# Performance work log

Hardware: AMD Instinct MI355X
Metric: run time of the kernel (lower is better)

Reference implementation:

```python
import math
import jax, jax.numpy as jnp
import numpy as np

B, S, D, H = 4, 2048, 1024, 16
HD = D // H
SAMPLING_FACTOR = 5.0


def setup_inputs() -> dict:
    key = jax.random.key(0)
    ks = jax.random.split(key, 6)
    std = 1.0 / math.sqrt(D)
    inp = {
        "x": jax.random.normal(ks[0], (B, S, D), dtype=jnp.float32),
        "Wq": jax.random.normal(ks[1], (D, D), dtype=jnp.float32) * std,
        "bq": jnp.zeros((D,), dtype=jnp.float32),
        "Wk": jax.random.normal(ks[2], (D, D), dtype=jnp.float32) * std,
        "bk": jnp.zeros((D,), dtype=jnp.float32),
        "Wv": jax.random.normal(ks[3], (D, D), dtype=jnp.float32) * std,
        "bv": jnp.zeros((D,), dtype=jnp.float32),
        "Wo": jax.random.normal(ks[4], (D, D), dtype=jnp.float32) * std,
        "bo": jnp.zeros((D,), dtype=jnp.float32),
        "sample_idx": jax.random.randint(ks[5], (S,), 0, S, dtype=jnp.int32),
    }
    return inp


def reference(x, Wq, bq, Wk, bk, Wv, bv, Wo, bo, sample_idx):
    batch, seq_len, d_model = x.shape
    scale = math.sqrt(HD)
    # u = number of top (active) queries; U_part = seq_len here (sampling saturates)
    u = max(1, min(seq_len, int(SAMPLING_FACTOR * math.log(seq_len + 1))))

    def proj(W, b):
        # [B,S,D] -> [B,H,S,hd]
        return (x @ W + b).reshape(batch, seq_len, H, HD).transpose(0, 2, 1, 3)

    Q = proj(Wq, bq)
    K = proj(Wk, bk)
    V = proj(Wv, bv)

    # sparsity measure over sampled keys (with replacement)
    K_sample = K[:, :, sample_idx, :]                     # [B,H,U,hd]
    scores_sample = jnp.einsum("bhsd,bhud->bhsu", Q, K_sample) / scale
    M = scores_sample.max(axis=-1) - scores_sample.mean(axis=-1)  # [B,H,S]

    _, top_idx = jax.lax.top_k(M, u)                      # [B,H,u]

    Q_reduce = jnp.take_along_axis(Q, top_idx[..., None], axis=2)  # [B,H,u,hd]
    attn_scores = jnp.einsum("bhud,bhsd->bhus", Q_reduce, K) / scale
    attn_probs = jax.nn.softmax(attn_scores, axis=-1)
    context = jnp.einsum("bhus,bhsd->bhud", attn_probs, V)        # [B,H,u,hd]

    # fill lazy queries with mean of V, scatter active-query contexts
    V_mean = V.mean(axis=2, keepdims=True)                # [B,H,1,hd]
    out = jnp.broadcast_to(V_mean, (batch, H, seq_len, HD))
    b_idx = jnp.arange(batch)[:, None, None]
    h_idx = jnp.arange(H)[None, :, None]
    out = out.at[b_idx, h_idx, top_idx].set(context)      # [B,H,S,hd]

    out = out.transpose(0, 2, 1, 3).reshape(batch, seq_len, d_model)
    return out @ Wo + bo
```

## Files before the change

### kernel.cpp

```cpp
#include <hip/hip_runtime.h>
#include <math.h>
#include <stdint.h>
#include <stddef.h>

#define BB 4
#define SS 2048
#define DD 1024
#define HH 16
#define HD 64
#define UU 38
#define BH (BB*HH)
#define NROWS (BB*SS)
#define QSZ (BB*HH*SS*HD)
#define NSPLIT 4
#define SPLEN (SS/NSPLIT)
#define QPAD 40

typedef unsigned short ushortT;
typedef unsigned int u32;
typedef __attribute__((ext_vector_type(8))) short bf16x8;
typedef __attribute__((ext_vector_type(4))) float f32x4;

static __device__ __forceinline__ ushortT f2bf(float f) {
  union { float f; unsigned int u; } v; v.f = f;
  unsigned int r = v.u + 0x7fffu + ((v.u >> 16) & 1u);
  return (ushortT)(r >> 16);
}
static __device__ __forceinline__ float bf2f(ushortT h) {
  union { unsigned int u; float f; } v; v.u = ((unsigned int)h) << 16; return v.f;
}
static __device__ __forceinline__ void gld16(const void* g, void* l) {
  __builtin_amdgcn_global_load_lds((const __attribute__((address_space(1))) u32*)g,
                                   (__attribute__((address_space(3))) u32*)l, 16, 0, 0);
}

__global__ __launch_bounds__(256) void split_x(
    const float* __restrict__ x, ushortT* __restrict__ xh, ushortT* __restrict__ xl)
{
  size_t i = ((size_t)blockIdx.x * 256 + threadIdx.x) * 8;
  float4 v0 = *(const float4*)&x[i];
  float4 v1 = *(const float4*)&x[i + 4];
  float fv[8] = {v0.x, v0.y, v0.z, v0.w, v1.x, v1.y, v1.z, v1.w};
  bf16x8 hv, lv;
#pragma unroll
  for (int j = 0; j < 8; ++j) {
    ushortT h = f2bf(fv[j]);
    hv[j] = (short)h;
    lv[j] = (short)f2bf(fv[j] - bf2f(h));
  }
  *(bf16x8*)&xh[i] = hv;
  *(bf16x8*)&xl[i] = lv;
}

__global__ __launch_bounds__(256) void splitT_kernel(
    const float* __restrict__ W, ushortT* __restrict__ WhT, ushortT* __restrict__ WlT)
{
  __shared__ float tile[64][65];
  const int t = threadIdx.x;
  const int bk = blockIdx.y * 64, bn = blockIdx.x * 64;
  const int rr = t >> 4, c4 = (t & 15) * 4;
#pragma unroll
  for (int p = 0; p < 4; ++p) {
    int row = rr + p * 16;
    float4 v = *(const float4*)&W[(size_t)(bk + row) * DD + bn + c4];
    tile[row][c4] = v.x; tile[row][c4+1] = v.y; tile[row][c4+2] = v.z; tile[row][c4+3] = v.w;
  }
  __syncthreads();
  const int n = t & 63, ks = (t >> 6) * 16;
  union { ushortT us[16]; uint4 q[2]; } hb, lb;
#pragma unroll
  for (int j = 0; j < 16; ++j) {
    float f = tile[ks + j][n];
    ushortT h = f2bf(f);
    hb.us[j] = h;
    lb.us[j] = f2bf(f - bf2f(h));
  }
  size_t o = ((size_t)(bn + n) * DD + (size_t)(bk + ks)) >> 3;
  ((uint4*)WhT)[o] = hb.q[0]; ((uint4*)WhT)[o + 1] = hb.q[1];
  ((uint4*)WlT)[o] = lb.q[0]; ((uint4*)WlT)[o + 1] = lb.q[1];
}

__global__ __launch_bounds__(256) void dedupe_kernel(
    const int* __restrict__ sidx, int* __restrict__ uidx, int* __restrict__ ucount)
{
  __shared__ unsigned bm[64];
  __shared__ int base[64];
  const int t = threadIdx.x;
  if (t < 64) bm[t] = 0;
  __syncthreads();
  for (int s = t; s < SS; s += 256) {
    int v = sidx[s];
    atomicOr(&bm[v >> 5], 1u << (v & 31));
  }
  __syncthreads();
  if (t < 64) {
    int c = __popc(bm[t]);
    int pre = c;
#pragma unroll
    for (int off = 1; off < 64; off <<= 1) {
      int o = __shfl_up(pre, off, 64);
      if (t >= off) pre += o;
    }
    base[t] = pre - c;
    if (t == 63) ucount[0] = pre;
  }
  __syncthreads();
  if (t < 64) {
    unsigned m = bm[t];
    int o = base[t];
    while (m) {
      int b = __ffs(m) - 1;
      uidx[o++] = t * 32 + b;
      m &= m - 1;
    }
  }
  __syncthreads();
  int total = ucount[0];
  int padded = (total + 127) & ~127;
  int first = uidx[0];
  for (int i = total + t; i < padded; i += 256) uidx[i] = first;
}

template<bool EMIT_B16, bool EMIT_F32>
__global__ __launch_bounds__(256, 3) void gemm_mfma(
    const ushortT* __restrict__ Axh, const ushortT* __restrict__ Axl,
    const ushortT* __restrict__ BhT, const ushortT* __restrict__ BlT,
    const float* __restrict__ bias,
    float* __restrict__ outF, ushortT* __restrict__ outH, ushortT* __restrict__ outL)
{
  __shared__ ushortT As[128 * 64];
  __shared__ ushortT Bs[128 * 64];
  const int t = threadIdx.x;
  const int lin = blockIdx.x;
  const int swz = (lin & 7) * 64 + (lin >> 3);
  const int m0 = (swz >> 3) * 128;
  const int n0 = (swz & 7) * 128;
  const int lane = t & 63, w = t >> 6;
  const int wr = w >> 1, wc = w & 1;
  const int fr = lane & 15, fs = lane >> 4;
  const int srow = t >> 3, sslot = t & 7;
  f32x4 acc[4][4];
#pragma unroll
  for (int i = 0; i < 4; ++i)
#pragma unroll
    for (int j = 0; j < 4; ++j) acc[i][j] = (f32x4){0.f, 0.f, 0.f, 0.f};

  for (int kt = 0; kt < 48; ++kt) {
    const int seg = kt >> 4;
    const int rk0 = (kt & 15) * 64;
    const ushortT* a_src = (seg == 1) ? Axl : Axh;
    const ushortT* b_src = (seg == 2) ? BlT : BhT;
    __syncthreads();
#pragma unroll
    for (int is = 0; is < 4; ++is) {
      int row = is * 32 + srow;
      int soff = ((sslot ^ (row & 7)) * 8);
      int cb = (is * 256 + (t & 192)) * 8;
      gld16(&a_src[(size_t)(m0 + row) * DD + rk0 + soff], &As[cb]);
      gld16(&b_src[(size_t)(n0 + row) * DD + rk0 + soff], &Bs[cb]);
    }
    __syncthreads();
#pragma unroll
    for (int kk = 0; kk < 2; ++kk) {
      bf16x8 af[4], bf[4];
#pragma unroll
      for (int i = 0; i < 4; ++i) {
        int row = wr * 64 + i * 16 + fr;
        af[i] = *(const bf16x8*)&As[row * 64 + (((kk * 4 + fs) ^ (row & 7)) * 8)];
      }
#pragma unroll
      for (int j = 0; j < 4; ++j) {
        int row = wc * 64 + j * 16 + fr;
        bf[j] = *(const bf16x8*)&Bs[row * 64 + (((kk * 4 + fs) ^ (row & 7)) * 8)];
      }
#pragma unroll
      for (int i = 0; i < 4; ++i)
#pragma unroll
        for (int j = 0; j < 4; ++j)
          acc[i][j] = __builtin_amdgcn_mfma_f32_16x16x32_bf16(af[i], bf[j], acc[i][j], 0, 0, 0);
    }
  }
#pragma unroll
  for (int i = 0; i < 4; ++i) {
#pragma unroll
    for (int j = 0; j < 4; ++j) {
      int c = n0 + wc * 64 + j * 16 + fr;
      float bs = bias[c];
      int h = c >> 6, hd = c & 63;
#pragma unroll
      for (int r = 0; r < 4; ++r) {
        int m = m0 + wr * 64 + i * 16 + fs * 4 + r;
        int b = m >> 11, s = m & (SS - 1);
        size_t oidx = (((size_t)(b * HH + h)) * SS + s) * HD + hd;
        float val = acc[i][j][r] + bs;
        if (EMIT_F32) outF[oidx] = val;
        if (EMIT_B16) {
          ushortT hv = f2bf(val);
          outH[oidx] = hv;
          outL[oidx] = f2bf(val - bf2f(hv));
        }
      }
    }
  }
}

__global__ __launch_bounds__(256) void means_kernel(
    const float* __restrict__ K, const float* __restrict__ V,
    const int* __restrict__ sidx,
    float* __restrict__ Kmean, float* __restrict__ Vmean)
{
  __shared__ float rk[4][64], rv[4][64];
  const int bh = blockIdx.x;
  const int t = threadIdx.x;
  const int d = t & 63, p = t >> 6;
  const float* Kb = K + (size_t)bh * SS * HD;
  const float* Vb = V + (size_t)bh * SS * HD;
  float ka = 0.f, va = 0.f;
  for (int r = p * 512; r < (p + 1) * 512; ++r) {
    ka += Kb[(size_t)sidx[r] * HD + d];
    va += Vb[(size_t)r * HD + d];
  }
  rk[p][d] = ka; rv[p][d] = va;
  __syncthreads();
  if (t < 64) {
    Kmean[bh * HD + t] = (rk[0][t] + rk[1][t] + rk[2][t] + rk[3][t]) * (1.0f / SS);
    Vmean[bh * HD + t] = (rv[0][t] + rv[1][t] + rv[2][t] + rv[3][t]) * (1.0f / SS);
  }
}

__global__ __launch_bounds__(256, 2) void m_mfma(
    const ushortT* __restrict__ Qhg, const ushortT* __restrict__ Qlg,
    const ushortT* __restrict__ Khg, const ushortT* __restrict__ Klg,
    const int* __restrict__ uidx, const int* __restrict__ ucount,
    const float* __restrict__ Kmean, float* __restrict__ M)
{
  __shared__ ushortT QhL[128 * 64], QlL[128 * 64], KhL[128 * 64], KlL[128 * 64];
  __shared__ float Mred[2][128];
  __shared__ float km[64];
  const int t = threadIdx.x;
  const int lin = blockIdx.x;
  const int swz = (lin & 7) * 128 + (lin >> 3);
  const int bh = swz >> 4;
  const int s0 = (swz & 15) * 128;
  const int lane = t & 63, w = t >> 6;
  const int wr = w >> 1, wc = w & 1;
  const int fr = lane & 15, fs = lane >> 4;
  if (t < 64) km[t] = Kmean[bh * HD + t];
  const int srow = t >> 3, sslot = t & 7;
  const int ntiles = (ucount[0] + 127) >> 7;
#pragma unroll
  for (int is = 0; is < 4; ++is) {
    int row = is * 32 + srow;
    int soff = ((sslot ^ (row & 7)) * 8);
    int cb = (is * 256 + (t & 192)) * 8;
    size_t ga = ((size_t)bh * SS + s0 + row) * HD + soff;
    gld16(&Qhg[ga], &QhL[cb]);
    gld16(&Qlg[ga], &QlL[cb]);
  }
  float runmax[4][4];
#pragma unroll
  for (int i = 0; i < 4; ++i)
#pragma unroll
    for (int r = 0; r < 4; ++r) runmax[i][r] = -INFINITY;

  for (int ui = 0; ui < ntiles; ++ui) {
    __syncthreads();
#pragma unroll
    for (int is = 0; is < 4; ++is) {
      int row = is * 32 + srow;
      int gr = uidx[ui * 128 + row];
      int soff = ((sslot ^ (row & 7)) * 8);
      int cb = (is * 256 + (t & 192)) * 8;
      size_t ga = ((size_t)bh * SS + gr) * HD + soff;
      gld16(&Khg[ga], &KhL[cb]);
      gld16(&Klg[ga], &KlL[cb]);
    }
    __syncthreads();
    f32x4 acc[4][4];
#pragma unroll
    for (int i = 0; i < 4; ++i)
#pragma unroll
      for (int j = 0; j < 4; ++j) acc[i][j] = (f32x4){0.f, 0.f, 0.f, 0.f};
#pragma unroll
    for (int kk = 0; kk < 2; ++kk) {
      bf16x8 ah[4], al[4], bh[4], bl[4];
#pragma unroll
      for (int i = 0; i < 4; ++i) {
        int row = wr * 64 + i * 16 + fr;
        int off = row * 64 + (((kk * 4 + fs) ^ (row & 7)) * 8);
        ah[i] = *(const bf16x8*)&QhL[off];
        al[i] = *(const bf16x8*)&QlL[off];
      }
#pragma unroll
      for (int j = 0; j < 4; ++j) {
        int row = wc * 64 + j * 16 + fr;
        int off = row * 64 + (((kk * 4 + fs) ^ (row & 7)) * 8);
        bh[j] = *(const bf16x8*)&KhL[off];
        bl[j] = *(const bf16x8*)&KlL[off];
      }
#pragma unroll
      for (int i = 0; i < 4; ++i)
#pragma unroll
        for (int j = 0; j < 4; ++j) {
          acc[i][j] = __builtin_amdgcn_mfma_f32_16x16x32_bf16(ah[i], bh[j], acc[i][j], 0, 0, 0);
          acc[i][j] = __builtin_amdgcn_mfma_f32_16x16x32_bf16(ah[i], bl[j], acc[i][j], 0, 0, 0);
          acc[i][j] = __builtin_amdgcn_mfma_f32_16x16x32_bf16(al[i], bh[j], acc[i][j], 0, 0, 0);
        }
    }
#pragma unroll
    for (int i = 0; i < 4; ++i)
#pragma unroll
      for (int j = 0; j < 4; ++j)
#pragma unroll
        for (int r = 0; r < 4; ++r) runmax[i][r] = fmaxf(runmax[i][r], acc[i][j][r]);
  }
#pragma unroll
  for (int i = 0; i < 4; ++i)
#pragma unroll
    for (int r = 0; r < 4; ++r) {
      float v = runmax[i][r];
      v = fmaxf(v, __shfl_xor(v, 1, 64));
      v = fmaxf(v, __shfl_xor(v, 2, 64));
      v = fmaxf(v, __shfl_xor(v, 4, 64));
      v = fmaxf(v, __shfl_xor(v, 8, 64));
      runmax[i][r] = v;
    }
  if (fr == 0) {
#pragma unroll
    for (int i = 0; i < 4; ++i)
#pragma unroll
      for (int r = 0; r < 4; ++r)
        Mred[wc][wr * 64 + i * 16 + fs * 4 + r] = runmax[i][r];
  }
  __syncthreads();
  if (t < 128) {
    float mx = fmaxf(Mred[0][t], Mred[1][t]);
    float md = 0.f;
    const ushortT* qh = &Qhg[((size_t)bh * SS + s0 + t) * HD];
    const ushortT* ql = &Qlg[((size_t)bh * SS + s0 + t) * HD];
#pragma unroll
    for (int k8 = 0; k8 < 8; ++k8) {
      bf16x8 hv = *(const bf16x8*)&qh[k8 * 8];
      bf16x8 lv = *(const bf16x8*)&ql[k8 * 8];
#pragma unroll
      for (int j = 0; j < 8; ++j)
        md += (bf2f((ushortT)hv[j]) + bf2f((ushortT)lv[j])) * km[k8 * 8 + j];
    }
    M[(size_t)bh * SS + s0 + t] = (mx - md) * 0.125f;
  }
}

__global__ __launch_bounds__(256) void topk_kernel(const float* __restrict__ M,
                                                   int* __restrict__ topi)
{
  __shared__ float rw[4];
  __shared__ int   ri4[4];
  __shared__ int   winner;
  const int t = threadIdx.x, bh = blockIdx.x;
  const int lane = t & 63, w = t >> 6;
  float v[8];
#pragma unroll
  for (int j = 0; j < 8; ++j) v[j] = M[(size_t)bh * SS + t + j * 256];
  for (int it = 0; it < UU; ++it) {
    float bv = v[0]; int bj = 0;
#pragma unroll
    for (int j = 1; j < 8; ++j) if (v[j] > bv) { bv = v[j]; bj = j; }
    int bs = t + bj * 256;
#pragma unroll
    for (int off = 32; off > 0; off >>= 1) {
      float ov = __shfl_xor(bv, off, 64);
      int os = __shfl_xor(bs, off, 64);
      if (ov > bv || (ov == bv && os < bs)) { bv = ov; bs = os; }
    }
    if (lane == 0) { rw[w] = bv; ri4[w] = bs; }
    __syncthreads();
    if (t == 0) {
      float fv = rw[0]; int fsx = ri4[0];
#pragma unroll
      for (int g = 1; g < 4; ++g)
        if (rw[g] > fv || (rw[g] == fv && ri4[g] < fsx)) { fv = rw[g]; fsx = ri4[g]; }
      topi[bh * UU + it] = fsx;
      winner = fsx;
    }
    __syncthreads();
    int wi = winner;
    if ((wi & 255) == t) {
      int jj = wi >> 8;
#pragma unroll
      for (int j = 0; j < 8; ++j) if (j == jj) v[j] = -INFINITY;
    }
  }
}

__global__ __launch_bounds__(256) void attn_flash(
    const ushortT* __restrict__ Qhg, const ushortT* __restrict__ Qlg,
    const float* __restrict__ K, const float* __restrict__ V,
    const int* __restrict__ topi,
    float* __restrict__ pacc, float* __restrict__ pm, float* __restrict__ pl)
{
  __shared__ float Qt[64][68];
  __shared__ float KV[64][68];
  __shared__ float Ps[64][68];
  __shared__ float redA[16][64];
  __shared__ float redB[16][64];
  __shared__ float mrow[64], lrow[64], scl[64];
  const int t  = threadIdx.x;
  const int bh = blockIdx.x;
  const int sp = blockIdx.y;
  const float* Kb = K + (size_t)bh * SS * HD;
  const float* Vb = V + (size_t)bh * SS * HD;
  if (t < 64) { mrow[t] = -INFINITY; lrow[t] = 0.f; }
  {
    int q = t >> 2, k4 = (t & 3) * 16;
    float fv[16];
#pragma unroll
    for (int e = 0; e < 16; ++e) fv[e] = 0.f;
    if (q < UU) {
      int qidx = topi[bh * UU + q];
      size_t ga = ((size_t)bh * SS + qidx) * HD + k4;
      bf16x8 h0 = *(const bf16x8*)&Qhg[ga];
      bf16x8 h1 = *(const bf16x8*)&Qhg[ga + 8];
      bf16x8 l0 = *(const bf16x8*)&Qlg[ga];
      bf16x8 l1 = *(const bf16x8*)&Qlg[ga + 8];
#pragma unroll
      for (int j = 0; j < 8; ++j) {
        fv[j]     = bf2f((ushortT)h0[j]) + bf2f((ushortT)l0[j]);
        fv[8 + j] = bf2f((ushortT)h1[j]) + bf2f((ushortT)l1[j]);
      }
    }
#pragma unroll
    for (int e = 0; e < 16; ++e) Qt[k4 + e][q] = fv[e];
  }
  const int q4 = (t & 15) * 4, j4g = (t >> 4) * 4, d4 = (t >> 4) * 4;
  const int lj = t >> 2, lk4 = (t & 3) * 16;
  float acc[4][4] = {};
  for (int s0 = sp * SPLEN; s0 < (sp + 1) * SPLEN; s0 += 64) {
    __syncthreads();
#pragma unroll
    for (int i = 0; i < 4; ++i) {
      float4 v = *(const float4*)&Kb[(size_t)(s0 + lj) * HD + lk4 + 4 * i];
      KV[lk4 + 4*i + 0][lj] = v.x; KV[lk4 + 4*i + 1][lj] = v.y;
      KV[lk4 + 4*i + 2][lj] = v.z; KV[lk4 + 4*i + 3][lj] = v.w;
    }
    __syncthreads();
    float sacc[4][4] = {};
#pragma unroll 16
    for (int k = 0; k < 64; ++k) {
      float4 a = *(const float4*)&Qt[k][q4];
      float4 b = *(const float4*)&KV[k][j4g];
      sacc[0][0] += a.x*b.x; sacc[0][1] += a.x*b.y; sacc[0][2] += a.x*b.z; sacc[0][3] += a.x*b.w;
      sacc[1][0] += a.y*b.x; sacc[1][1] += a.y*b.y; sacc[1][2] += a.y*b.z; sacc[1][3] += a.y*b.w;
      sacc[2][0] += a.z*b.x; sacc[2][1] += a.z*b.y; sacc[2][2] += a.z*b.z; sacc[2][3] += a.z*b.w;
      sacc[3][0] += a.w*b.x; sacc[3][1] += a.w*b.y; sacc[3][2] += a.w*b.z; sacc[3][3] += a.w*b.w;
    }
#pragma unroll
    for (int i = 0; i < 4; ++i) {
      float mx = fmaxf(fmaxf(sacc[i][0], sacc[i][1]), fmaxf(sacc[i][2], sacc[i][3]));
      redA[t >> 4][q4 + i] = mx;
    }
    __syncthreads();
    if (t < 64) {
      float mx = redA[0][t];
#pragma unroll
      for (int g = 1; g < 16; ++g) mx = fmaxf(mx, redA[g][t]);
      float mn = fmaxf(mrow[t], mx * 0.125f);
      scl[t] = __expf(mrow[t] - mn);
      mrow[t] = mn;
    }
    __syncthreads();
    float4 vld[4];
#pragma unroll
    for (int i = 0; i < 4; ++i)
      vld[i] = *(const float4*)&Vb[(size_t)(s0 + lj) * HD + lk4 + 4 * i];
    float psum[4] = {};
#pragma unroll
    for (int i = 0; i < 4; ++i) {
#pragma unroll
      for (int j = 0; j < 4; ++j) {
        float e = __expf(sacc[i][j] * 0.125f - mrow[q4 + i]);
        Ps[j4g + j][q4 + i] = e;
        psum[i] += e;
      }
      redB[t >> 4][q4 + i] = psum[i];
    }
#pragma unroll
    for (int i = 0; i < 4; ++i)
      *(float4*)&KV[lj][lk4 + 4 * i] = vld[i];
    __syncthreads();
    if (t < 64) {
      float ts = redB[0][t];
#pragma unroll
      for (int g = 1; g < 16; ++g) ts += redB[g][t];
      lrow[t] = lrow[t] * scl[t] + ts;
    }
#pragma unroll
    for (int i = 0; i < 4; ++i) {
      float fsc = scl[q4 + i];
      acc[i][0] *= fsc; acc[i][1] *= fsc; acc[i][2] *= fsc; acc[i][3] *= fsc;
    }
#pragma unroll 16
    for (int j = 0; j < 64; ++j) {
      float4 a = *(const float4*)&Ps[j][q4];
      float4 b = *(const float4*)&KV[j][d4];
      acc[0][0] += a.x*b.x; acc[0][1] += a.x*b.y; acc[0][2] += a.x*b.z; acc[0][3] += a.x*b.w;
      acc[1][0] += a.y*b.x; acc[1][1] += a.y*b.y; acc[1][2] += a.y*b.z; acc[1][3] += a.y*b.w;
      acc[2][0] += a.z*b.x; acc[2][1] += a.z*b.y; acc[2][2] += a.z*b.z; acc[2][3] += a.z*b.w;
      acc[3][0] += a.w*b.x; acc[3][1] += a.w*b.y; acc[3][2] += a.w*b.z; acc[3][3] += a.w*b.w;
    }
  }
  const size_t pb = ((size_t)bh * NSPLIT + sp) * QPAD;
#pragma unroll
  for (int i = 0; i < 4; ++i) {
    int q = q4 + i;
    if (q < UU) {
#pragma unroll
      for (int j = 0; j < 4; ++j)
        pacc[(pb + q) * HD + d4 + j] = acc[i][j];
    }
  }
  if (t < UU) { pm[pb + t] = mrow[t]; pl[pb + t] = lrow[t]; }
}

__global__ __launch_bounds__(256) void attn_combine(
    const float* __restrict__ pacc, const float* __restrict__ pm,
    const float* __restrict__ pl, float* __restrict__ ctx)
{
  const int t  = threadIdx.x;
  const int bh = blockIdx.x;
  const int d = t & 63, qg = t >> 6;
  for (int q = qg; q < UU; q += 4) {
    float m0 = pm[((size_t)bh * NSPLIT + 0) * QPAD + q];
    float m1 = pm[((size_t)bh * NSPLIT + 1) * QPAD + q];
    float m2 = pm[((size_t)bh * NSPLIT + 2) * QPAD + q];
    float m3 = pm[((size_t)bh * NSPLIT + 3) * QPAD + q];
    float ms = fmaxf(fmaxf(m0, m1), fmaxf(m2, m3));
    float w0 = __expf(m0 - ms), w1 = __expf(m1 - ms), w2 = __expf(m2 - ms), w3 = __expf(m3 - ms);
    float l = w0 * pl[((size_t)bh * NSPLIT + 0) * QPAD + q]
            + w1 * pl[((size_t)bh * NSPLIT + 1) * QPAD + q]
            + w2 * pl[((size_t)bh * NSPLIT + 2) * QPAD + q]
            + w3 * pl[((size_t)bh * NSPLIT + 3) * QPAD + q];
    float c = w0 * pacc[(((size_t)bh * NSPLIT + 0) * QPAD + q) * HD + d]
            + w1 * pacc[(((size_t)bh * NSPLIT + 1) * QPAD + q) * HD + d]
            + w2 * pacc[(((size_t)bh * NSPLIT + 2) * QPAD + q) * HD + d]
            + w3 * pacc[(((size_t)bh * NSPLIT + 3) * QPAD + q) * HD + d];
    ctx[((size_t)bh * UU + q) * HD + d] = c / l;
  }
}

__global__ void base_kernel(const float* __restrict__ Vmean, const float* __restrict__ Wo,
                            const float* __restrict__ bo, float* __restrict__ base)
{
  const int c = blockIdx.x * 256 + threadIdx.x;
  float acc[BB] = {};
  for (int k = 0; k < DD; ++k) {
    float w = Wo[(size_t)k * DD + c];
#pragma unroll
    for (int b = 0; b < BB; ++b) acc[b] += Vmean[b * DD + k] * w;
  }
#pragma unroll
  for (int b = 0; b < BB; ++b) base[b * DD + c] = acc[b] + bo[c];
}

__global__ void fill_kernel(const float* __restrict__ base, float* __restrict__ out)
{
  size_t i = (size_t)blockIdx.x * 256 + threadIdx.x;
  float4 bv = ((const float4*)base)[(i >> 19) * 256 + (i & 255)];
  ((float4*)out)[i] = bv;
}

__global__ __launch_bounds__(256) void scatter_kernel(
    const float* __restrict__ ctx, const float* __restrict__ Vmean,
    const int* __restrict__ topi, const float* __restrict__ Wo,
    float* __restrict__ out)
{
  __shared__ float delta[64];
  const int t  = threadIdx.x;
  const int bh = blockIdx.x;
  const int u  = blockIdx.y;
  const int b = bh >> 4, h = bh & 15;
  const int s = topi[bh * UU + u];
  if (t < 64) delta[t] = ctx[((size_t)bh * UU + u) * HD + t] - Vmean[bh * HD + t];
  __syncthreads();
  float* orow = out + ((size_t)b * SS + s) * DD;
#pragma unroll
  for (int j = 0; j < 4; ++j) {
    int c = t + j * 256;
    float acc = 0.f;
#pragma unroll 8
    for (int d = 0; d < 64; ++d) acc += delta[d] * Wo[(size_t)(h * HD + d) * DD + c];
    atomicAdd(&orow[c], acc);
  }
}

extern "C" void kernel_launch(void* const* d_in, const int* in_sizes, int n_in,
                              void* d_out, int out_size, void* d_ws, size_t ws_size,
                              hipStream_t stream) {
  const float* x  = (const float*)d_in[0];
  const float* Wq = (const float*)d_in[1];
  const float* bq = (const float*)d_in[2];
  const float* Wk = (const float*)d_in[3];
  const float* bk = (const float*)d_in[4];
  const float* Wv = (const float*)d_in[5];
  const float* bv = (const float*)d_in[6];
  const float* Wo = (const float*)d_in[7];
  const float* bo = (const float*)d_in[8];
  const int* sidx = (const int*)d_in[9];
  float* out = (float*)d_out;

  float* f     = (float*)d_ws;
  float* K     = f;
  float* V     = f + (size_t)QSZ;
  float* Kmean = f + (size_t)2 * QSZ;
  float* Vmean = Kmean + BH * HD;
  float* Mbuf  = Vmean + BH * HD;
  float* base  = Mbuf + (size_t)BH * SS;
  float* ctx   = base + BB * DD;
  float* pacc  = ctx + (size_t)BH * UU * HD;
  float* pm    = pacc + (size_t)BH * NSPLIT * QPAD * HD;
  float* pl    = pm + (size_t)BH * NSPLIT * QPAD;
  int*   topi  = (int*)(pl + (size_t)BH * NSPLIT * QPAD);
  int*   uidx  = topi + 4096;
  int*   ucount= uidx + 4096;
  ushortT* usp = (ushortT*)(ucount + 64);
  ushortT* WqhT = usp;
  ushortT* WqlT = WqhT + (size_t)DD * DD;
  ushortT* WkhT = WqlT + (size_t)DD * DD;
  ushortT* WklT = WkhT + (size_t)DD * DD;
  ushortT* WvhT = WklT + (size_t)DD * DD;
  ushortT* WvlT = WvhT + (size_t)DD * DD;
  ushortT* xh   = WvlT + (size_t)DD * DD;
  ushortT* xl   = xh + (size_t)NROWS * DD;
  ushortT* Qhg  = xl + (size_t)NROWS * DD;
  ushortT* Qlg  = Qhg + (size_t)QSZ;
  ushortT* Khg  = Qlg + (size_t)QSZ;
  ushortT* Klg  = Khg + (size_t)QSZ;

  split_x<<<NROWS * DD / (256 * 8), 256, 0, stream>>>(x, xh, xl);
  dim3 gs(16, 16);
  splitT_kernel<<<gs, 256, 0, stream>>>(Wq, WqhT, WqlT);
  splitT_kernel<<<gs, 256, 0, stream>>>(Wk, WkhT, WklT);
  splitT_kernel<<<gs, 256, 0, stream>>>(Wv, WvhT, WvlT);
  dedupe_kernel<<<1, 256, 0, stream>>>(sidx, uidx, ucount);
  gemm_mfma<true, false><<<512, 256, 0, stream>>>(xh, xl, WqhT, WqlT, bq, nullptr, Qhg, Qlg);
  gemm_mfma<true, true ><<<512, 256, 0, stream>>>(xh, xl, WkhT, WklT, bk, K, Khg, Klg);
  gemm_mfma<false, true><<<512, 256, 0, stream>>>(xh, xl, WvhT, WvlT, bv, V, nullptr, nullptr);
  means_kernel<<<BH, 256, 0, stream>>>(K, V, sidx, Kmean, Vmean);
  m_mfma<<<1024, 256, 0, stream>>>(Qhg, Qlg, Khg, Klg, uidx, ucount, Kmean, Mbuf);
  topk_kernel<<<BH, 256, 0, stream>>>(Mbuf, topi);
  attn_flash<<<dim3(BH, NSPLIT), 256, 0, stream>>>(Qhg, Qlg, K, V, topi, pacc, pm, pl);
  attn_combine<<<BH, 256, 0, stream>>>(pacc, pm, pl, ctx);
  base_kernel<<<DD / 256, 256, 0, stream>>>(Vmean, Wo, bo, base);
  fill_kernel<<<(NROWS * DD / 4) / 256, 256, 0, stream>>>(base, out);
  scatter_kernel<<<dim3(BH, UU), 256, 0, stream>>>(ctx, Vmean, topi, Wo, out);
}
```

Before: 473.3 us.

## Fuse QKV GEMMs, drop fp32 K, split attention finer, parallelize base GEMV

The three projection GEMM launches become a single 1536-block kernel that selects weights, bias and output by tile index. K is no longer written in fp32; the means and attention kernels rebuild it from the bf16 hi/lo pair, which saves one large fp32 write. The attention split count goes from 4 to 8 for more blocks, with a generic combine loop. The base GEMV now splits the k-loop across threads and reduces through shared memory, giving 64 blocks instead of 4.

New measurement: 474.8 us. No clear change (+0.3%).

```diff
diff --git a/kernel.cpp b/kernel.cpp
--- a/kernel.cpp
+++ b/kernel.cpp
@@ -12,7 +12,7 @@
 #define BH (BB*HH)
 #define NROWS (BB*SS)
 #define QSZ (BB*HH*SS*HD)
-#define NSPLIT 4
+#define NSPLIT 8
 #define SPLEN (SS/NSPLIT)
 #define QPAD 40
 
@@ -121,20 +121,28 @@
   for (int i = total + t; i < padded; i += 256) uidx[i] = first;
 }
 
-template<bool EMIT_B16, bool EMIT_F32>
-__global__ __launch_bounds__(256, 3) void gemm_mfma(
+__global__ __launch_bounds__(256, 3) void gemm_qkv(
     const ushortT* __restrict__ Axh, const ushortT* __restrict__ Axl,
-    const ushortT* __restrict__ BhT, const ushortT* __restrict__ BlT,
-    const float* __restrict__ bias,
-    float* __restrict__ outF, ushortT* __restrict__ outH, ushortT* __restrict__ outL)
+    const ushortT* __restrict__ WqhT, const ushortT* __restrict__ WqlT,
+    const ushortT* __restrict__ WkhT, const ushortT* __restrict__ WklT,
+    const ushortT* __restrict__ WvhT, const ushortT* __restrict__ WvlT,
+    const float* __restrict__ bq, const float* __restrict__ bk, const float* __restrict__ bv,
+    ushortT* __restrict__ Qhg, ushortT* __restrict__ Qlg,
+    ushortT* __restrict__ Khg, ushortT* __restrict__ Klg,
+    float* __restrict__ V)
 {
   __shared__ ushortT As[128 * 64];
   __shared__ ushortT Bs[128 * 64];
   const int t = threadIdx.x;
   const int lin = blockIdx.x;
-  const int swz = (lin & 7) * 64 + (lin >> 3);
-  const int m0 = (swz >> 3) * 128;
-  const int n0 = (swz & 7) * 128;
+  const int swz = (lin & 7) * 192 + (lin >> 3);
+  const int n_idx = swz >> 6;
+  const int m0 = (swz & 63) * 128;
+  const int p = n_idx >> 3;
+  const int n0 = (n_idx & 7) * 128;
+  const ushortT* Bh = (p == 0) ? WqhT : (p == 1) ? WkhT : WvhT;
+  const ushortT* Bl = (p == 0) ? WqlT : (p == 1) ? WklT : WvlT;
+  const float* bias = (p == 0) ? bq : (p == 1) ? bk : bv;
   const int lane = t & 63, w = t >> 6;
   const int wr = w >> 1, wc = w & 1;
   const int fr = lane & 15, fs = lane >> 4;
@@ -149,7 +157,7 @@
     const int seg = kt >> 4;
     const int rk0 = (kt & 15) * 64;
     const ushortT* a_src = (seg == 1) ? Axl : Axh;
-    const ushortT* b_src = (seg == 2) ? BlT : BhT;
+    const ushortT* b_src = (seg == 2) ? Bl : Bh;
     __syncthreads();
 #pragma unroll
     for (int is = 0; is < 4; ++is) {
@@ -193,11 +201,13 @@
         int b = m >> 11, s = m & (SS - 1);
         size_t oidx = (((size_t)(b * HH + h)) * SS + s) * HD + hd;
         float val = acc[i][j][r] + bs;
-        if (EMIT_F32) outF[oidx] = val;
-        if (EMIT_B16) {
+        if (p == 2) {
+          V[oidx] = val;
+        } else {
           ushortT hv = f2bf(val);
-          outH[oidx] = hv;
-          outL[oidx] = f2bf(val - bf2f(hv));
+          ushortT lv = f2bf(val - bf2f(hv));
+          if (p == 0) { Qhg[oidx] = hv; Qlg[oidx] = lv; }
+          else        { Khg[oidx] = hv; Klg[oidx] = lv; }
         }
       }
     }
@@ -205,19 +215,19 @@
 }
 
 __global__ __launch_bounds__(256) void means_kernel(
-    const float* __restrict__ K, const float* __restrict__ V,
-    const int* __restrict__ sidx,
+    const ushortT* __restrict__ Khg, const ushortT* __restrict__ Klg,
+    const float* __restrict__ V, const int* __restrict__ sidx,
     float* __restrict__ Kmean, float* __restrict__ Vmean)
 {
   __shared__ float rk[4][64], rv[4][64];
   const int bh = blockIdx.x;
   const int t = threadIdx.x;
   const int d = t & 63, p = t >> 6;
-  const float* Kb = K + (size_t)bh * SS * HD;
   const float* Vb = V + (size_t)bh * SS * HD;
   float ka = 0.f, va = 0.f;
   for (int r = p * 512; r < (p + 1) * 512; ++r) {
-    ka += Kb[(size_t)sidx[r] * HD + d];
+    size_t ki = ((size_t)bh * SS + sidx[r]) * HD + d;
+    ka += bf2f(Khg[ki]) + bf2f(Klg[ki]);
     va += Vb[(size_t)r * HD + d];
   }
   rk[p][d] = ka; rv[p][d] = va;
@@ -394,8 +404,8 @@
 
 __global__ __launch_bounds__(256) void attn_flash(
     const ushortT* __restrict__ Qhg, const ushortT* __restrict__ Qlg,
-    const float* __restrict__ K, const float* __restrict__ V,
-    const int* __restrict__ topi,
+    const ushortT* __restrict__ Khg, const ushortT* __restrict__ Klg,
+    const float* __restrict__ V, const int* __restrict__ topi,
     float* __restrict__ pacc, float* __restrict__ pm, float* __restrict__ pl)
 {
   __shared__ float Qt[64][68];
@@ -407,7 +417,6 @@
   const int t  = threadIdx.x;
   const int bh = blockIdx.x;
   const int sp = blockIdx.y;
-  const float* Kb = K + (size_t)bh * SS * HD;
   const float* Vb = V + (size_t)bh * SS * HD;
   if (t < 64) { mrow[t] = -INFINITY; lrow[t] = 0.f; }
   {
@@ -436,11 +445,17 @@
   float acc[4][4] = {};
   for (int s0 = sp * SPLEN; s0 < (sp + 1) * SPLEN; s0 += 64) {
     __syncthreads();
-#pragma unroll
-    for (int i = 0; i < 4; ++i) {
-      float4 v = *(const float4*)&Kb[(size_t)(s0 + lj) * HD + lk4 + 4 * i];
-      KV[lk4 + 4*i + 0][lj] = v.x; KV[lk4 + 4*i + 1][lj] = v.y;
-      KV[lk4 + 4*i + 2][lj] = v.z; KV[lk4 + 4*i + 3][lj] = v.w;
+    {
+      size_t ga = ((size_t)bh * SS + s0 + lj) * HD + lk4;
+      bf16x8 h0 = *(const bf16x8*)&Khg[ga];
+      bf16x8 h1 = *(const bf16x8*)&Khg[ga + 8];
+      bf16x8 l0 = *(const bf16x8*)&Klg[ga];
+      bf16x8 l1 = *(const bf16x8*)&Klg[ga + 8];
+#pragma unroll
+      for (int j = 0; j < 8; ++j) {
+        KV[lk4 + j][lj]     = bf2f((ushortT)h0[j]) + bf2f((ushortT)l0[j]);
+        KV[lk4 + 8 + j][lj] = bf2f((ushortT)h1[j]) + bf2f((ushortT)l1[j]);
+      }
     }
     __syncthreads();
     float sacc[4][4] = {};
@@ -529,36 +544,48 @@
   const int bh = blockIdx.x;
   const int d = t & 63, qg = t >> 6;
   for (int q = qg; q < UU; q += 4) {
-    float m0 = pm[((size_t)bh * NSPLIT + 0) * QPAD + q];
-    float m1 = pm[((size_t)bh * NSPLIT + 1) * QPAD + q];
-    float m2 = pm[((size_t)bh * NSPLIT + 2) * QPAD + q];
-    float m3 = pm[((size_t)bh * NSPLIT + 3) * QPAD + q];
-    float ms = fmaxf(fmaxf(m0, m1), fmaxf(m2, m3));
-    float w0 = __expf(m0 - ms), w1 = __expf(m1 - ms), w2 = __expf(m2 - ms), w3 = __expf(m3 - ms);
-    float l = w0 * pl[((size_t)bh * NSPLIT + 0) * QPAD + q]
-            + w1 * pl[((size_t)bh * NSPLIT + 1) * QPAD + q]
-            + w2 * pl[((size_t)bh * NSPLIT + 2) * QPAD + q]
-            + w3 * pl[((size_t)bh * NSPLIT + 3) * QPAD + q];
-    float c = w0 * pacc[(((size_t)bh * NSPLIT + 0) * QPAD + q) * HD + d]
-            + w1 * pacc[(((size_t)bh * NSPLIT + 1) * QPAD + q) * HD + d]
-            + w2 * pacc[(((size_t)bh * NSPLIT + 2) * QPAD + q) * HD + d]
-            + w3 * pacc[(((size_t)bh * NSPLIT + 3) * QPAD + q) * HD + d];
+    float mv[NSPLIT];
+    float ms = -INFINITY;
+#pragma unroll
+    for (int sp = 0; sp < NSPLIT; ++sp) {
+      mv[sp] = pm[((size_t)bh * NSPLIT + sp) * QPAD + q];
+      ms = fmaxf(ms, mv[sp]);
+    }
+    float l = 0.f, c = 0.f;
+#pragma unroll
+    for (int sp = 0; sp < NSPLIT; ++sp) {
+      float wv = __expf(mv[sp] - ms);
+      l += wv * pl[((size_t)bh * NSPLIT + sp) * QPAD + q];
+      c += wv * pacc[(((size_t)bh * NSPLIT + sp) * QPAD + q) * HD + d];
+    }
     ctx[((size_t)bh * UU + q) * HD + d] = c / l;
   }
 }
 
-__global__ void base_kernel(const float* __restrict__ Vmean, const float* __restrict__ Wo,
-                            const float* __restrict__ bo, float* __restrict__ base)
-{
-  const int c = blockIdx.x * 256 + threadIdx.x;
+__global__ __launch_bounds__(256) void base_kernel(
+    const float* __restrict__ Vmean, const float* __restrict__ Wo,
+    const float* __restrict__ bo, float* __restrict__ base)
+{
+  __shared__ float red[16][BB][16];
+  const int t = threadIdx.x;
+  const int cl = t & 15, kg = t >> 4;
+  const int c = blockIdx.x * 16 + cl;
   float acc[BB] = {};
-  for (int k = 0; k < DD; ++k) {
+  for (int k = kg * 64; k < kg * 64 + 64; ++k) {
     float w = Wo[(size_t)k * DD + c];
 #pragma unroll
     for (int b = 0; b < BB; ++b) acc[b] += Vmean[b * DD + k] * w;
   }
 #pragma unroll
-  for (int b = 0; b < BB; ++b) base[b * DD + c] = acc[b] + bo[c];
+  for (int b = 0; b < BB; ++b) red[kg][b][cl] = acc[b];
+  __syncthreads();
+  if (t < 64) {
+    int b = t >> 4, cc = blockIdx.x * 16 + (t & 15);
+    float s = 0.f;
+#pragma unroll
+    for (int g = 0; g < 16; ++g) s += red[g][b][t & 15];
+    base[b * DD + cc] = s + bo[cc];
+  }
 }
 
 __global__ void fill_kernel(const float* __restrict__ base, float* __restrict__ out)
@@ -608,9 +635,8 @@
   float* out = (float*)d_out;
 
   float* f     = (float*)d_ws;
-  float* K     = f;
-  float* V     = f + (size_t)QSZ;
-  float* Kmean = f + (size_t)2 * QSZ;
+  float* V     = f;
+  float* Kmean = f + (size_t)QSZ;
   float* Vmean = Kmean + BH * HD;
   float* Mbuf  = Vmean + BH * HD;
   float* base  = Mbuf + (size_t)BH * SS;
@@ -641,15 +667,14 @@
   splitT_kernel<<<gs, 256, 0, stream>>>(Wk, WkhT, WklT);
   splitT_kernel<<<gs, 256, 0, stream>>>(Wv, WvhT, WvlT);
   dedupe_kernel<<<1, 256, 0, stream>>>(sidx, uidx, ucount);
-  gemm_mfma<true, false><<<512, 256, 0, stream>>>(xh, xl, WqhT, WqlT, bq, nullptr, Qhg, Qlg);
-  gemm_mfma<true, true ><<<512, 256, 0, stream>>>(xh, xl, WkhT, WklT, bk, K, Khg, Klg);
-  gemm_mfma<false, true><<<512, 256, 0, stream>>>(xh, xl, WvhT, WvlT, bv, V, nullptr, nullptr);
-  means_kernel<<<BH, 256, 0, stream>>>(K, V, sidx, Kmean, Vmean);
+  gemm_qkv<<<1536, 256, 0, stream>>>(xh, xl, WqhT, WqlT, WkhT, WklT, WvhT, WvlT,
+                                     bq, bk, bv, Qhg, Qlg, Khg, Klg, V);
+  means_kernel<<<BH, 256, 0, stream>>>(Khg, Klg, V, sidx, Kmean, Vmean);
   m_mfma<<<1024, 256, 0, stream>>>(Qhg, Qlg, Khg, Klg, uidx, ucount, Kmean, Mbuf);
   topk_kernel<<<BH, 256, 0, stream>>>(Mbuf, topi);
-  attn_flash<<<dim3(BH, NSPLIT), 256, 0, stream>>>(Qhg, Qlg, K, V, topi, pacc, pm, pl);
+  attn_flash<<<dim3(BH, NSPLIT), 256, 0, stream>>>(Qhg, Qlg, Khg, Klg, V, topi, pacc, pm, pl);
   attn_combine<<<BH, 256, 0, stream>>>(pacc, pm, pl, ctx);
-  base_kernel<<<DD / 256, 256, 0, stream>>>(Vmean, Wo, bo, base);
+  base_kernel<<<DD / 16, 256, 0, stream>>>(Vmean, Wo, bo, base);
   fill_kernel<<<(NROWS * DD / 4) / 256, 256, 0, stream>>>(base, out);
   scatter_kernel<<<dim3(BH, UU), 256, 0, stream>>>(ctx, Vmean, topi, Wo, out);
 }
```
